# Kernel tuning notes

Hardware: AMD Instinct MI355X
Metric: run time of the kernel (lower is better)

## Reference

```python
import jax, jax.numpy as jnp
import numpy as np

# dims: S slots, B batch, D pred-rep dim, E slot-embedding dim, H hidden/output dim, V per-slot vocab
S, B, D, E, H, V = 7, 4096, 1024, 128, 512, 200
D0 = D + E  # layer-0 LSTM input size


def setup_inputs() -> dict:
    key = jax.random.key(0)
    ks = jax.random.split(key, 12)
    rn = lambda k, shape, s=0.02: jax.random.normal(k, shape, jnp.float32) * s
    return {
        "pred_reps": jax.random.normal(ks[0], (B, D), jnp.float32),
        "slot_labels": jax.random.randint(ks[1], (S, B), 0, V),
        "emb": rn(ks[2], (S, V, E), 1.0),
        # layer 0: per-slot LSTMCell + highway params
        "Wih0": rn(ks[3], (S, 4 * H, D0)), "Whh0": rn(ks[4], (S, 4 * H, H)),
        "bih0": jnp.zeros((S, 4 * H), jnp.float32), "bhh0": jnp.zeros((S, 4 * H), jnp.float32),
        "hwW0": rn(ks[5], (S, H, D0 + H)), "hwb0": jnp.zeros((S, H), jnp.float32),
        "linW0": rn(ks[6], (S, H, D0)),
        # layer 1 (input size = H)
        "Wih1": rn(ks[7], (S, 4 * H, H)), "Whh1": rn(ks[8], (S, 4 * H, H)),
        "bih1": jnp.zeros((S, 4 * H), jnp.float32), "bhh1": jnp.zeros((S, 4 * H), jnp.float32),
        "hwW1": rn(ks[9], (S, H, 2 * H)), "hwb1": jnp.zeros((S, H), jnp.float32),
        "linW1": rn(ks[10], (S, H, H)),
    }


def _lstm_cell(x, h, c, Wih, Whh, bih, bhh):
    # torch LSTMCell: gates ordered i, f, g, o
    gates = x @ Wih.T + bih + h @ Whh.T + bhh
    i, f, g, o = jnp.split(gates, 4, axis=-1)
    c_new = jax.nn.sigmoid(f) * c + jax.nn.sigmoid(i) * jnp.tanh(g)
    h_new = jax.nn.sigmoid(o) * jnp.tanh(c_new)
    return h_new, c_new


def reference(pred_reps, slot_labels, emb, Wih0, Whh0, bih0, bhh0, hwW0, hwb0, linW0,
              Wih1, Whh1, bih1, bhh1, hwW1, hwb1, linW1):
    def step(carry, xs):
        h0, c0, h1, c1 = carry
        (tbl, idx, wih0, whh0, bi0, bh0, hw0, hb0, lw0,
         wih1, whh1, bi1, bh1, hw1, hb1, lw1) = xs
        # per-slot embedding gather + concat with predicate reps  -> [B, D0]
        x = jnp.concatenate([pred_reps, tbl[idx]], axis=-1)
        # layer 0 cell + highway gate
        h0n, c0n = _lstm_cell(x, h0, c0, wih0, whh0, bi0, bh0)
        gate0 = jax.nn.sigmoid(jnp.concatenate([x, h0n], axis=-1) @ hw0.T + hb0)
        x1 = gate0 * h0n + (1.0 - gate0) * (x @ lw0.T)
        # layer 1 cell (its highway output is dead code in the original: curr_input
        # after the last layer is discarded, so we skip it -- same math)
        h1n, c1n = _lstm_cell(x1, h1, c1, wih1, whh1, bi1, bh1)
        return (h0n, c0n, h1n, c1n), None

    init = tuple(jnp.zeros((B, H), pred_reps.dtype) for _ in range(4))
    xs = (emb, slot_labels, Wih0, Whh0, bih0, bhh0, hwW0, hwb0, linW0,
          Wih1, Whh1, bih1, bhh1, hwW1, hwb1, linW1)
    carry, _ = jax.lax.scan(step, init, xs)
    return carry[2]  # last_h: top-layer hidden after final slot
```

## Files before the change

kernel.cpp:

```cpp
#include <hip/hip_runtime.h>
#include <stdint.h>

typedef unsigned short u16;

#define S_   7
#define B_   4096
#define D_   1024
#define E_   128
#define H_   512
#define V_   200
#define D0_  1152
#define KX0  1664
#define KX1  1024
#define G4H  2048

typedef __bf16 bf16x8 __attribute__((ext_vector_type(8)));
typedef float  f32x4  __attribute__((ext_vector_type(4)));
typedef u16    u16x8  __attribute__((ext_vector_type(8)));

__device__ __forceinline__ u16 f2bf(float f) {
  union { float f; uint32_t u; } v; v.f = f;
  uint32_t r = v.u + 0x7fffu + ((v.u >> 16) & 1u);
  return (u16)(r >> 16);
}
__device__ __forceinline__ float bf2f(u16 b) {
  union { uint32_t u; float f; } v; v.u = ((uint32_t)b) << 16;
  return v.f;
}
__device__ __forceinline__ float sigmoidf_(float x) { return 1.0f / (1.0f + __expf(-x)); }
__device__ __forceinline__ float tanhf_(float x) {
  float t = __expf(-2.f * fabsf(x));
  return copysignf((1.f - t) / (1.f + t), x);
}

__device__ __forceinline__ void glds16(const u16* g, u16* l) {
  __builtin_amdgcn_global_load_lds(
      (const __attribute__((address_space(1))) uint32_t*)g,
      (__attribute__((address_space(3))) uint32_t*)l, 16, 0, 0);
}

__global__ void pack8(const float* __restrict__ A, int ka,
                      u16* __restrict__ dst, int kk) {
  int k8 = (blockIdx.x * 256 + threadIdx.x) * 8;
  long row = blockIdx.y;
  if (k8 >= kk) return;
  float v[8];
  if (k8 + 8 <= ka) {
    const float4* p = (const float4*)(A + row * ka + k8);
    float4 x = p[0], y = p[1];
    v[0]=x.x; v[1]=x.y; v[2]=x.z; v[3]=x.w; v[4]=y.x; v[5]=y.y; v[6]=y.z; v[7]=y.w;
  } else {
    #pragma unroll
    for (int j = 0; j < 8; ++j) v[j] = 0.f;
  }
  u16x8 o;
  #pragma unroll
  for (int j = 0; j < 8; ++j) o[j] = f2bf(v[j]);
  *(u16x8*)&dst[row * kk + k8] = o;
}

__global__ void pack_gates(const float* __restrict__ Wih, int ka,
                           const float* __restrict__ Whh, int kb,
                           u16* __restrict__ dst, int kk) {
  int k8 = (blockIdx.x * 256 + threadIdx.x) * 8;
  if (k8 >= kk) return;
  long sr = blockIdx.y;
  long s = sr >> 11;
  int  r = (int)(sr & 2047);
  int  g = r >> 9, j = r & 511;
  long drow = (s << 11) + ((j >> 4) * 64 + g * 16 + (j & 15));
  float v[8];
  if (k8 + 8 <= ka) {
    const float4* p = (const float4*)(Wih + sr * ka + k8);
    float4 x = p[0], y = p[1];
    v[0]=x.x; v[1]=x.y; v[2]=x.z; v[3]=x.w; v[4]=y.x; v[5]=y.y; v[6]=y.z; v[7]=y.w;
  } else {
    const float4* p = (const float4*)(Whh + sr * kb + (k8 - ka));
    float4 x = p[0], y = p[1];
    v[0]=x.x; v[1]=x.y; v[2]=x.z; v[3]=x.w; v[4]=y.x; v[5]=y.y; v[6]=y.z; v[7]=y.w;
  }
  u16x8 o;
  #pragma unroll
  for (int q = 0; q < 8; ++q) o[q] = f2bf(v[q]);
  *(u16x8*)&dst[drow * kk + k8] = o;
}

__global__ void pack_hl(const float* __restrict__ src, int ks,
                        u16* __restrict__ dst, int kk, int off16) {
  int k8 = (blockIdx.x * 256 + threadIdx.x) * 8;
  if (k8 >= kk) return;
  long sj = blockIdx.y;
  long s = sj >> 9;
  int  j = (int)(sj & 511);
  long drow = (s << 10) + ((j >> 4) * 32 + off16 + (j & 15));
  float v[8];
  if (k8 + 8 <= ks) {
    const float4* p = (const float4*)(src + sj * ks + k8);
    float4 x = p[0], y = p[1];
    v[0]=x.x; v[1]=x.y; v[2]=x.z; v[3]=x.w; v[4]=y.x; v[5]=y.y; v[6]=y.z; v[7]=y.w;
  } else {
    #pragma unroll
    for (int q = 0; q < 8; ++q) v[q] = 0.f;
  }
  u16x8 o;
  #pragma unroll
  for (int q = 0; q < 8; ++q) o[q] = f2bf(v[q]);
  *(u16x8*)&dst[drow * kk + k8] = o;
}

__global__ void bias_sum(const float* __restrict__ a, const float* __restrict__ b,
                         float* __restrict__ o, int n) {
  int i = blockIdx.x * 256 + threadIdx.x;
  if (i < n) o[i] = a[i] + b[i];
}

__global__ void zero_f(float* __restrict__ p, int n) {
  for (int i = blockIdx.x * 256 + threadIdx.x; i < n; i += gridDim.x * 256) p[i] = 0.f;
}
__global__ void zero_u16k(u16* __restrict__ p, int n) {
  for (int i = blockIdx.x * 256 + threadIdx.x; i < n; i += gridDim.x * 256) p[i] = 0;
}

__global__ void gather_emb(const float* __restrict__ emb_s, const int* __restrict__ idx_s,
                           u16* __restrict__ xcat) {
  long b = blockIdx.x;
  int e = threadIdx.x;
  int ix = idx_s[b];
  xcat[b * KX0 + D_ + e] = f2bf(emb_s[(long)ix * E_ + e]);
}

template<int MODE>
__global__ __launch_bounds__(256)
void gemm_fused(const u16* __restrict__ A, int lda,
                const u16* __restrict__ W, int ldw,
                int K, int ntn, int cpx,
                const float* __restrict__ bsum,
                float* __restrict__ cbuf,
                u16* __restrict__ hdst, int hld, int hoff,
                float* __restrict__ hf32,
                const u16* __restrict__ xcat0) {
  __shared__ __align__(16) u16 lds[2 * 2 * 128 * 64];
  const int BUFSZ = 2 * 128 * 64;
  const int tid  = threadIdx.x;
  const int lane = tid & 63;
  const int wave = tid >> 6;
  const int p    = blockIdx.x;
  const int bid  = (p & 7) * cpx + (p >> 3);
  const int tn = bid % ntn;
  const int tm = bid / ntn;
  const long row0 = (long)tm * 128;
  const long col0 = (long)tn * 128;
  const int wm = (wave >> 1) * 64;
  const int wn = (wave & 1) * 64;
  const int fr = lane & 15;
  const int fk = (lane >> 4) * 8;
  const int wr = wave * 32;

  const int srow = wr + (lane >> 3);
  const int scol = ((lane & 7) ^ ((lane >> 3) & 7)) * 8;
  const u16* ga = A + (row0 + srow) * (long)lda + scol;
  const u16* gw = W + (col0 + srow) * (long)ldw + scol;
  u16* dstA = &lds[0] + wr * 64 + lane * 8;
  u16* dstW = dstA + 128 * 64;

  int aoff[4], woff[4];
  #pragma unroll
  for (int m = 0; m < 4; ++m) aoff[m] = (wm + m * 16 + fr) * 64;
  #pragma unroll
  for (int n = 0; n < 4; ++n) woff[n] = (wn + n * 16 + fr) * 64 + 128 * 64;
  const int swz = (fr & 7) << 3;
  const int kk0 = (0 + fk) ^ swz;
  const int kk1 = (32 + fk) ^ swz;

  f32x4 acc[4][4] = {};
  const int nt = K >> 6;

  #pragma unroll
  for (int i = 0; i < 4; ++i) {
    glds16(ga + (long)(i * 8) * lda, dstA + i * 512);
    glds16(gw + (long)(i * 8) * ldw, dstW + i * 512);
  }

  int cur = 0;
  for (int t = 0; t < nt; ++t) {
    __syncthreads();
    if (t + 1 < nt) {
      const long k0 = (long)(t + 1) << 6;
      const int nb = (cur ^ 1) * BUFSZ;
      #pragma unroll
      for (int i = 0; i < 4; ++i) {
        glds16(ga + (long)(i * 8) * lda + k0, dstA + nb + i * 512);
        glds16(gw + (long)(i * 8) * ldw + k0, dstW + nb + i * 512);
      }
    }
    const u16* base = &lds[cur * BUFSZ];
    bf16x8 af0[4], wf0[4], af1[4], wf1[4];
    #pragma unroll
    for (int m = 0; m < 4; ++m) af0[m] = *(const bf16x8*)&base[aoff[m] + kk0];
    #pragma unroll
    for (int n = 0; n < 4; ++n) wf0[n] = *(const bf16x8*)&base[woff[n] + kk0];
    #pragma unroll
    for (int m = 0; m < 4; ++m) af1[m] = *(const bf16x8*)&base[aoff[m] + kk1];
    #pragma unroll
    for (int n = 0; n < 4; ++n) wf1[n] = *(const bf16x8*)&base[woff[n] + kk1];
    #pragma unroll
    for (int m = 0; m < 4; ++m)
      #pragma unroll
      for (int n = 0; n < 4; ++n)
        acc[m][n] = __builtin_amdgcn_mfma_f32_16x16x32_bf16(af0[m], wf0[n], acc[m][n], 0, 0, 0);
    #pragma unroll
    for (int m = 0; m < 4; ++m)
      #pragma unroll
      for (int n = 0; n < 4; ++n)
        acc[m][n] = __builtin_amdgcn_mfma_f32_16x16x32_bf16(af1[m], wf1[n], acc[m][n], 0, 0, 0);
    cur ^= 1;
  }

  const int cr = (lane >> 4) * 4;
  const int jg = wn >> 6;

  if (MODE == 0) {
    const int j = tn * 32 + jg * 16 + fr;
    const float bi = bsum[j], bf = bsum[512 + j], bg = bsum[1024 + j], bo = bsum[1536 + j];
    #pragma unroll
    for (int m = 0; m < 4; ++m) {
      const long rbase = row0 + wm + m * 16 + cr;
      #pragma unroll
      for (int r = 0; r < 4; ++r) {
        const long ri = rbase + r;
        float gi = acc[m][0][r] + bi;
        float gf = acc[m][1][r] + bf;
        float gg = acc[m][2][r] + bg;
        float go = acc[m][3][r] + bo;
        float cv = cbuf[ri * H_ + j];
        float cn = sigmoidf_(gf) * cv + sigmoidf_(gi) * tanhf_(gg);
        float hn = sigmoidf_(go) * tanhf_(cn);
        cbuf[ri * H_ + j] = cn;
        hdst[ri * hld + hoff + j] = f2bf(hn);
        if (hf32) hf32[ri * H_ + j] = hn;
      }
    }
  } else {
    #pragma unroll
    for (int pp = 0; pp < 2; ++pp) {
      const int j = tn * 64 + jg * 32 + pp * 16 + fr;
      const float bj = bsum[j];
      #pragma unroll
      for (int m = 0; m < 4; ++m) {
        const long rbase = row0 + wm + m * 16 + cr;
        #pragma unroll
        for (int r = 0; r < 4; ++r) {
          const long ri = rbase + r;
          float gv = sigmoidf_(acc[m][2 * pp][r] + bj);
          float h0 = bf2f(xcat0[ri * KX0 + D0_ + j]);
          float x1 = gv * h0 + (1.f - gv) * acc[m][2 * pp + 1][r];
          hdst[ri * hld + hoff + j] = f2bf(x1);
        }
      }
    }
  }
}

extern "C" void kernel_launch(void* const* d_in, const int* in_sizes, int n_in,
                              void* d_out, int out_size, void* d_ws, size_t ws_size,
                              hipStream_t stream) {
  const float* pred   = (const float*)d_in[0];
  const int*   labels = (const int*)d_in[1];
  const float* emb    = (const float*)d_in[2];
  const float* Wih0   = (const float*)d_in[3];
  const float* Whh0   = (const float*)d_in[4];
  const float* bih0   = (const float*)d_in[5];
  const float* bhh0   = (const float*)d_in[6];
  const float* hwW0   = (const float*)d_in[7];
  const float* hwb0   = (const float*)d_in[8];
  const float* linW0  = (const float*)d_in[9];
  const float* Wih1   = (const float*)d_in[10];
  const float* Whh1   = (const float*)d_in[11];
  const float* bih1   = (const float*)d_in[12];
  const float* bhh1   = (const float*)d_in[13];
  float* out = (float*)d_out;

  char* ws = (char*)d_ws;
  size_t off = 0;
  auto alloc = [&](size_t bytes) {
    char* p = ws + off;
    off = (off + bytes + 255) & ~(size_t)255;
    return p;
  };
  u16* WC0   = (u16*)alloc((size_t)S_ * G4H * KX0 * 2);
  u16* WHL   = (u16*)alloc((size_t)S_ * 1024 * KX0 * 2);
  u16* WC1   = (u16*)alloc((size_t)S_ * G4H * KX1 * 2);
  u16* xcat  = (u16*)alloc((size_t)B_ * KX0 * 2);
  u16* x1cat = (u16*)alloc((size_t)B_ * KX1 * 2);
  float* c0   = (float*)alloc((size_t)B_ * H_ * 4);
  float* c1   = (float*)alloc((size_t)B_ * H_ * 4);
  float* bs0  = (float*)alloc((size_t)S_ * G4H * 4);
  float* bs1  = (float*)alloc((size_t)S_ * G4H * 4);

  pack_gates<<<dim3(1, S_ * G4H), 256, 0, stream>>>(Wih0, D0_, Whh0, H_, WC0, KX0);
  pack_gates<<<dim3(1, S_ * G4H), 256, 0, stream>>>(Wih1, H_, Whh1, H_, WC1, KX1);
  pack_hl<<<dim3(1, S_ * H_), 256, 0, stream>>>(hwW0, KX0, WHL, KX0, 0);
  pack_hl<<<dim3(1, S_ * H_), 256, 0, stream>>>(linW0, D0_, WHL, KX0, 16);
  pack8<<<dim3(1, B_), 256, 0, stream>>>(pred, D_, xcat, KX0);
  bias_sum<<<(S_ * G4H + 255) / 256, 256, 0, stream>>>(bih0, bhh0, bs0, S_ * G4H);
  bias_sum<<<(S_ * G4H + 255) / 256, 256, 0, stream>>>(bih1, bhh1, bs1, S_ * G4H);
  zero_f<<<256, 256, 0, stream>>>(c0, B_ * H_);
  zero_f<<<256, 256, 0, stream>>>(c1, B_ * H_);
  zero_u16k<<<256, 256, 0, stream>>>(x1cat, B_ * KX1);

  const int g0 = (B_ / 128) * (G4H / 128);
  const int g1 = (B_ / 128) * (1024 / 128);

  for (int s = 0; s < S_; ++s) {
    gather_emb<<<B_, E_, 0, stream>>>(emb + (size_t)s * V_ * E_, labels + (size_t)s * B_, xcat);

    gemm_fused<0><<<g0, 256, 0, stream>>>(
        xcat, KX0, WC0 + (size_t)s * G4H * KX0, KX0, KX0, G4H / 128, g0 / 8,
        bs0 + (size_t)s * G4H, c0, xcat, KX0, D0_, nullptr, nullptr);

    gemm_fused<1><<<g1, 256, 0, stream>>>(
        xcat, KX0, WHL + (size_t)s * 1024 * KX0, KX0, KX0, 1024 / 128, g1 / 8,
        hwb0 + (size_t)s * H_, nullptr, x1cat, KX1, 0, nullptr, xcat);

    gemm_fused<0><<<g0, 256, 0, stream>>>(
        x1cat, KX1, WC1 + (size_t)s * G4H * KX1, KX1, KX1, G4H / 128, g0 / 8,
        bs1 + (size_t)s * G4H, c1, x1cat, KX1, H_, out, nullptr);
  }
}
```

Before: 681.0 us.

## Triple-buffer weight tiles in GEMM and flatten pack kernels with 4x work per thread

```diff
diff --git a/kernel.cpp b/kernel.cpp
--- a/kernel.cpp
+++ b/kernel.cpp
@@ -39,73 +39,94 @@
       (__attribute__((address_space(3))) uint32_t*)l, 16, 0, 0);
 }
 
-__global__ void pack8(const float* __restrict__ A, int ka,
-                      u16* __restrict__ dst, int kk) {
-  int k8 = (blockIdx.x * 256 + threadIdx.x) * 8;
-  long row = blockIdx.y;
-  if (k8 >= kk) return;
-  float v[8];
-  if (k8 + 8 <= ka) {
-    const float4* p = (const float4*)(A + row * ka + k8);
+__device__ __forceinline__ void cvt8(const float* src, u16x8* dst) {
+  const float4* p = (const float4*)src;
+  float4 x = p[0], y = p[1];
+  u16x8 o;
+  o[0]=f2bf(x.x); o[1]=f2bf(x.y); o[2]=f2bf(x.z); o[3]=f2bf(x.w);
+  o[4]=f2bf(y.x); o[5]=f2bf(y.y); o[6]=f2bf(y.z); o[7]=f2bf(y.w);
+  *dst = o;
+}
+
+template<int KA, int KB, int KK>
+__global__ void pack_gates4(const float* __restrict__ Wih, const float* __restrict__ Whh,
+                            u16* __restrict__ dst) {
+  const int NG = KK / 8;
+  const int stride = gridDim.x * 256;
+  int idx = blockIdx.x * 256 + threadIdx.x;
+  long daddr[4]; const float* saddr[4];
+  #pragma unroll
+  for (int u = 0; u < 4; ++u) {
+    int i = idx + u * stride;
+    int sr = i / NG, kg = i - sr * NG;
+    int k8 = kg * 8;
+    long s = sr >> 11;
+    int  r = sr & 2047;
+    int  g = r >> 9, j = r & 511;
+    long drow = (s << 11) + ((j >> 4) * 64 + g * 16 + (j & 15));
+    daddr[u] = drow * KK + k8;
+    saddr[u] = (k8 + 8 <= KA) ? (Wih + (long)sr * KA + k8)
+                              : (Whh + (long)sr * KB + (k8 - KA));
+  }
+  float v[4][8];
+  #pragma unroll
+  for (int u = 0; u < 4; ++u) {
+    const float4* p = (const float4*)saddr[u];
     float4 x = p[0], y = p[1];
-    v[0]=x.x; v[1]=x.y; v[2]=x.z; v[3]=x.w; v[4]=y.x; v[5]=y.y; v[6]=y.z; v[7]=y.w;
-  } else {
-    #pragma unroll
-    for (int j = 0; j < 8; ++j) v[j] = 0.f;
-  }
-  u16x8 o;
-  #pragma unroll
-  for (int j = 0; j < 8; ++j) o[j] = f2bf(v[j]);
-  *(u16x8*)&dst[row * kk + k8] = o;
-}
-
-__global__ void pack_gates(const float* __restrict__ Wih, int ka,
-                           const float* __restrict__ Whh, int kb,
-                           u16* __restrict__ dst, int kk) {
-  int k8 = (blockIdx.x * 256 + threadIdx.x) * 8;
-  if (k8 >= kk) return;
-  long sr = blockIdx.y;
-  long s = sr >> 11;
-  int  r = (int)(sr & 2047);
-  int  g = r >> 9, j = r & 511;
-  long drow = (s << 11) + ((j >> 4) * 64 + g * 16 + (j & 15));
-  float v[8];
-  if (k8 + 8 <= ka) {
-    const float4* p = (const float4*)(Wih + sr * ka + k8);
-    float4 x = p[0], y = p[1];
-    v[0]=x.x; v[1]=x.y; v[2]=x.z; v[3]=x.w; v[4]=y.x; v[5]=y.y; v[6]=y.z; v[7]=y.w;
-  } else {
-    const float4* p = (const float4*)(Whh + sr * kb + (k8 - ka));
-    float4 x = p[0], y = p[1];
-    v[0]=x.x; v[1]=x.y; v[2]=x.z; v[3]=x.w; v[4]=y.x; v[5]=y.y; v[6]=y.z; v[7]=y.w;
-  }
-  u16x8 o;
-  #pragma unroll
-  for (int q = 0; q < 8; ++q) o[q] = f2bf(v[q]);
-  *(u16x8*)&dst[drow * kk + k8] = o;
-}
-
-__global__ void pack_hl(const float* __restrict__ src, int ks,
-                        u16* __restrict__ dst, int kk, int off16) {
-  int k8 = (blockIdx.x * 256 + threadIdx.x) * 8;
-  if (k8 >= kk) return;
-  long sj = blockIdx.y;
-  long s = sj >> 9;
-  int  j = (int)(sj & 511);
-  long drow = (s << 10) + ((j >> 4) * 32 + off16 + (j & 15));
-  float v[8];
-  if (k8 + 8 <= ks) {
-    const float4* p = (const float4*)(src + sj * ks + k8);
-    float4 x = p[0], y = p[1];
-    v[0]=x.x; v[1]=x.y; v[2]=x.z; v[3]=x.w; v[4]=y.x; v[5]=y.y; v[6]=y.z; v[7]=y.w;
-  } else {
-    #pragma unroll
-    for (int q = 0; q < 8; ++q) v[q] = 0.f;
-  }
-  u16x8 o;
-  #pragma unroll
-  for (int q = 0; q < 8; ++q) o[q] = f2bf(v[q]);
-  *(u16x8*)&dst[drow * kk + k8] = o;
+    v[u][0]=x.x; v[u][1]=x.y; v[u][2]=x.z; v[u][3]=x.w;
+    v[u][4]=y.x; v[u][5]=y.y; v[u][6]=y.z; v[u][7]=y.w;
+  }
+  #pragma unroll
+  for (int u = 0; u < 4; ++u) {
+    u16x8 o;
+    #pragma unroll
+    for (int q = 0; q < 8; ++q) o[q] = f2bf(v[u][q]);
+    *(u16x8*)&dst[daddr[u]] = o;
+  }
+}
+
+template<int KS>
+__global__ void pack_hl4(const float* __restrict__ src, u16* __restrict__ dst, int off16) {
+  const int NG = KX0 / 8;
+  const int stride = gridDim.x * 256;
+  int idx = blockIdx.x * 256 + threadIdx.x;
+  #pragma unroll
+  for (int u = 0; u < 4; ++u) {
+    int i = idx + u * stride;
+    int sj = i / NG, kg = i - sj * NG;
+    int k8 = kg * 8;
+    long s = sj >> 9;
+    int  j = sj & 511;
+    long drow = (s << 10) + ((j >> 4) * 32 + off16 + (j & 15));
+    u16x8 o;
+    if (k8 + 8 <= KS) {
+      cvt8(src + (long)sj * KS + k8, &o);
+    } else {
+      #pragma unroll
+      for (int q = 0; q < 8; ++q) o[q] = 0;
+    }
+    *(u16x8*)&dst[drow * KX0 + k8] = o;
+  }
+}
+
+__global__ void pack_pred4(const float* __restrict__ pred, u16* __restrict__ dst) {
+  const int NG = KX0 / 8;
+  const int stride = gridDim.x * 256;
+  int idx = blockIdx.x * 256 + threadIdx.x;
+  #pragma unroll
+  for (int u = 0; u < 4; ++u) {
+    int i = idx + u * stride;
+    int row = i / NG, kg = i - row * NG;
+    int k8 = kg * 8;
+    u16x8 o;
+    if (k8 + 8 <= D_) {
+      cvt8(pred + (long)row * D_ + k8, &o);
+    } else {
+      #pragma unroll
+      for (int q = 0; q < 8; ++q) o[q] = 0;
+    }
+    *(u16x8*)&dst[(long)row * KX0 + k8] = o;
+  }
 }
 
 __global__ void bias_sum(const float* __restrict__ a, const float* __restrict__ b,
@@ -139,8 +160,9 @@
                 u16* __restrict__ hdst, int hld, int hoff,
                 float* __restrict__ hf32,
                 const u16* __restrict__ xcat0) {
-  __shared__ __align__(16) u16 lds[2 * 2 * 128 * 64];
-  const int BUFSZ = 2 * 128 * 64;
+  __shared__ __align__(16) u16 lds[(2 + 3) * 8192];
+  u16* lA = lds;
+  u16* lW = lds + 2 * 8192;
   const int tid  = threadIdx.x;
   const int lane = tid & 63;
   const int wave = tid >> 6;
@@ -160,14 +182,13 @@
   const int scol = ((lane & 7) ^ ((lane >> 3) & 7)) * 8;
   const u16* ga = A + (row0 + srow) * (long)lda + scol;
   const u16* gw = W + (col0 + srow) * (long)ldw + scol;
-  u16* dstA = &lds[0] + wr * 64 + lane * 8;
-  u16* dstW = dstA + 128 * 64;
+  const int dst0 = wr * 64 + lane * 8;
 
   int aoff[4], woff[4];
   #pragma unroll
   for (int m = 0; m < 4; ++m) aoff[m] = (wm + m * 16 + fr) * 64;
   #pragma unroll
-  for (int n = 0; n < 4; ++n) woff[n] = (wn + n * 16 + fr) * 64 + 128 * 64;
+  for (int n = 0; n < 4; ++n) woff[n] = (wn + n * 16 + fr) * 64;
   const int swz = (fr & 7) << 3;
   const int kk0 = (0 + fk) ^ swz;
   const int kk1 = (32 + fk) ^ swz;
@@ -175,34 +196,40 @@
   f32x4 acc[4][4] = {};
   const int nt = K >> 6;
 
-  #pragma unroll
-  for (int i = 0; i < 4; ++i) {
-    glds16(ga + (long)(i * 8) * lda, dstA + i * 512);
-    glds16(gw + (long)(i * 8) * ldw, dstW + i * 512);
-  }
-
-  int cur = 0;
+  auto stA = [&](int t, int b) {
+    const u16* g = ga + ((long)t << 6);
+    u16* d = lA + b * 8192 + dst0;
+    #pragma unroll
+    for (int i = 0; i < 4; ++i) glds16(g + (long)(i * 8) * lda, d + i * 512);
+  };
+  auto stW = [&](int t, int b) {
+    const u16* g = gw + ((long)t << 6);
+    u16* d = lW + b * 8192 + dst0;
+    #pragma unroll
+    for (int i = 0; i < 4; ++i) glds16(g + (long)(i * 8) * ldw, d + i * 512);
+  };
+
+  stA(0, 0);
+  stW(0, 0);
+  stW(1, 1);
+
   for (int t = 0; t < nt; ++t) {
-    __syncthreads();
-    if (t + 1 < nt) {
-      const long k0 = (long)(t + 1) << 6;
-      const int nb = (cur ^ 1) * BUFSZ;
-      #pragma unroll
-      for (int i = 0; i < 4; ++i) {
-        glds16(ga + (long)(i * 8) * lda + k0, dstA + nb + i * 512);
-        glds16(gw + (long)(i * 8) * ldw + k0, dstW + nb + i * 512);
-      }
-    }
-    const u16* base = &lds[cur * BUFSZ];
+    if (t + 1 < nt) asm volatile("s_waitcnt vmcnt(4)\n\ts_barrier" ::: "memory");
+    else            asm volatile("s_waitcnt vmcnt(0)\n\ts_barrier" ::: "memory");
+    if (t + 1 < nt) stA(t + 1, (t + 1) & 1);
+    if (t + 2 < nt) stW(t + 2, (t + 2) % 3);
+
+    const u16* Ab = lA + (t & 1) * 8192;
+    const u16* Wb = lW + (t % 3) * 8192;
     bf16x8 af0[4], wf0[4], af1[4], wf1[4];
     #pragma unroll
-    for (int m = 0; m < 4; ++m) af0[m] = *(const bf16x8*)&base[aoff[m] + kk0];
-    #pragma unroll
-    for (int n = 0; n < 4; ++n) wf0[n] = *(const bf16x8*)&base[woff[n] + kk0];
-    #pragma unroll
-    for (int m = 0; m < 4; ++m) af1[m] = *(const bf16x8*)&base[aoff[m] + kk1];
-    #pragma unroll
-    for (int n = 0; n < 4; ++n) wf1[n] = *(const bf16x8*)&base[woff[n] + kk1];
+    for (int m = 0; m < 4; ++m) af0[m] = *(const bf16x8*)&Ab[aoff[m] + kk0];
+    #pragma unroll
+    for (int n = 0; n < 4; ++n) wf0[n] = *(const bf16x8*)&Wb[woff[n] + kk0];
+    #pragma unroll
+    for (int m = 0; m < 4; ++m) af1[m] = *(const bf16x8*)&Ab[aoff[m] + kk1];
+    #pragma unroll
+    for (int n = 0; n < 4; ++n) wf1[n] = *(const bf16x8*)&Wb[woff[n] + kk1];
     #pragma unroll
     for (int m = 0; m < 4; ++m)
       #pragma unroll
@@ -213,7 +240,6 @@
       #pragma unroll
       for (int n = 0; n < 4; ++n)
         acc[m][n] = __builtin_amdgcn_mfma_f32_16x16x32_bf16(af1[m], wf1[n], acc[m][n], 0, 0, 0);
-    cur ^= 1;
   }
 
   const int cr = (lane >> 4) * 4;
@@ -297,11 +323,11 @@
   float* bs0  = (float*)alloc((size_t)S_ * G4H * 4);
   float* bs1  = (float*)alloc((size_t)S_ * G4H * 4);
 
-  pack_gates<<<dim3(1, S_ * G4H), 256, 0, stream>>>(Wih0, D0_, Whh0, H_, WC0, KX0);
-  pack_gates<<<dim3(1, S_ * G4H), 256, 0, stream>>>(Wih1, H_, Whh1, H_, WC1, KX1);
-  pack_hl<<<dim3(1, S_ * H_), 256, 0, stream>>>(hwW0, KX0, WHL, KX0, 0);
-  pack_hl<<<dim3(1, S_ * H_), 256, 0, stream>>>(linW0, D0_, WHL, KX0, 16);
-  pack8<<<dim3(1, B_), 256, 0, stream>>>(pred, D_, xcat, KX0);
+  pack_gates4<D0_, H_, KX0><<<2912, 256, 0, stream>>>(Wih0, Whh0, WC0);
+  pack_gates4<H_,  H_, KX1><<<1792, 256, 0, stream>>>(Wih1, Whh1, WC1);
+  pack_hl4<KX0><<<728, 256, 0, stream>>>(hwW0,  WHL, 0);
+  pack_hl4<D0_><<<728, 256, 0, stream>>>(linW0, WHL, 16);
+  pack_pred4<<<832, 256, 0, stream>>>(pred, xcat);
   bias_sum<<<(S_ * G4H + 255) / 256, 256, 0, stream>>>(bih0, bhh0, bs0, S_ * G4H);
   bias_sum<<<(S_ * G4H + 255) / 256, 256, 0, stream>>>(bih1, bhh1, bs1, S_ * G4H);
   zero_f<<<256, 256, 0, stream>>>(c0, B_ * H_);
```

Measured after the change: 698.2 us. 2.5% more time.
